# Performance work log

Measured on AMD Instinct MI355X. Metric: run time of the kernel, lower is better.

## Reference

```python
import jax, jax.numpy as jnp
import numpy as np

B, N, C = 16, 577, 768
H = 12
HD = C // H            # 64 head dim
F = HD // 2            # 32 rotary frequency pairs
END = 24               # sqrt(N - 1): patch grid side
SCALE = HD ** -0.5


def setup_inputs() -> dict:
    key = jax.random.key(0)
    k0, k1, k2, k3 = jax.random.split(key, 4)
    x = jax.random.normal(k0, (B, N, C), jnp.float32)
    qkv_w = jax.random.normal(k1, (3 * C, C), jnp.float32) * 0.02
    proj_w = jax.random.normal(k2, (C, C), jnp.float32) * 0.02
    proj_b = jnp.zeros((C,), jnp.float32)
    # learnable mixed 2D RoPE frequencies, [2, H*F] as in init_2d_freqs().view(2,-1)
    freqs = jax.random.normal(k3, (2, H * F), jnp.float32) * 0.5
    return {"x": x, "qkv_w": qkv_w, "proj_w": proj_w, "proj_b": proj_b, "freqs": freqs}


def _rope_angles(freqs):
    # compute_mixed_cis: per-head angle = t_x*fx + t_y*fy over the 24x24 grid
    t = jnp.arange(END * END, dtype=jnp.float32)
    t_x = t % END
    t_y = jnp.floor(t / END)
    ang = t_x[:, None] * freqs[0][None, :] + t_y[:, None] * freqs[1][None, :]  # [Np, H*F]
    return ang.reshape(END * END, H, F).transpose(1, 0, 2)  # [H, Np, F]


def _apply_rope(q, cos, sin):
    # q: [B,H,Np,HD] viewed as complex pairs [B,H,Np,F,2]; rotate by e^{i*ang}
    qp = q.reshape(*q.shape[:-1], F, 2)
    re, im = qp[..., 0], qp[..., 1]
    out = jnp.stack([re * cos - im * sin, re * sin + im * cos], axis=-1)
    return out.reshape(q.shape)


def reference(x, qkv_w, proj_w, proj_b, freqs):
    qkv = (x @ qkv_w.T).reshape(B, N, 3, H, HD).transpose(2, 0, 3, 1, 4)
    q, k, v = qkv[0], qkv[1], qkv[2]              # each [B,H,N,HD]
    ang = _rope_angles(freqs)                      # [H, Np, F]
    cos = jnp.cos(ang)[None]                       # [1,H,Np,F]
    sin = jnp.sin(ang)[None]
    # CLS token (index 0) bypasses RoPE
    q = jnp.concatenate([q[:, :, :1], _apply_rope(q[:, :, 1:], cos, sin)], axis=2)
    k = jnp.concatenate([k[:, :, :1], _apply_rope(k[:, :, 1:], cos, sin)], axis=2)
    attn = jax.nn.softmax((q * SCALE) @ jnp.swapaxes(k, -2, -1), axis=-1)  # [B,H,N,N]
    out = (attn @ v).transpose(0, 2, 1, 3).reshape(B, N, C)
    return out @ proj_w.T + proj_b
```

## Files before the change

### kernel.cpp

```cpp
#include <hip/hip_runtime.h>


typedef __bf16 bf16;
typedef __bf16 bf16x4 __attribute__((ext_vector_type(4)));
typedef __bf16 bf16x8 __attribute__((ext_vector_type(8)));
typedef float f32x4 __attribute__((ext_vector_type(4)));

namespace {
constexpr int kC = 768;
constexpr int kNtok = 577;
constexpr int kM = 16 * kNtok;
constexpr int kMpadQ = 9408;
constexpr int kMpadP = 9344;
constexpr int kTok = 640;
constexpr int kBH = 192;
}

typedef __attribute__((address_space(3))) unsigned int as3_u32;
typedef __attribute__((address_space(1))) unsigned int as1_u32;
__device__ __forceinline__ void gl16(const bf16* g, bf16* l) {
  __builtin_amdgcn_global_load_lds((const as1_u32*)g, (as3_u32*)l, 16, 0, 0);
}

__device__ __forceinline__ int swz_lid(int hid, int nwg) {
  int q = nwg >> 3, r = nwg & 7;
  int x = hid & 7, y = hid >> 3;
  int base = (x < r) ? x * (q + 1) : r * (q + 1) + (x - r) * q;
  return base + y;
}

__global__ __launch_bounds__(256) void prep_kernel(
    const float* __restrict__ x, const float* __restrict__ qkv_w,
    const float* __restrict__ proj_w, const float* __restrict__ freqs,
    bf16* __restrict__ xb, bf16* __restrict__ wqb, bf16* __restrict__ pwb,
    float* __restrict__ cosT, float* __restrict__ sinT) {
  const int bidx = (int)blockIdx.x;
  const int tid = (int)threadIdx.x;
  if (bidx < 3528) {
    int idx = bidx * 256 + tid;
    int m = idx / 96, c8 = (idx % 96) * 8;
    bf16x8 o;
    if (m < kM) {
      const float* p = x + (size_t)m * kC + c8;
#pragma unroll
      for (int j = 0; j < 8; ++j) o[j] = (bf16)p[j];
    } else {
#pragma unroll
      for (int j = 0; j < 8; ++j) o[j] = (bf16)0.0f;
    }
    *(bf16x8*)(xb + (size_t)m * kC + c8) = o;
  } else if (bidx < 3528 + 864) {
    int off = ((bidx - 3528) * 256 + tid) * 8;
    bf16x8 o;
#pragma unroll
    for (int j = 0; j < 8; ++j) o[j] = (bf16)qkv_w[off + j];
    *(bf16x8*)(wqb + off) = o;
  } else if (bidx < 3528 + 864 + 288) {
    int off = ((bidx - 3528 - 864) * 256 + tid) * 8;
    bf16x8 o;
#pragma unroll
    for (int j = 0; j < 8; ++j) o[j] = (bf16)proj_w[off + j];
    *(bf16x8*)(pwb + off) = o;
  } else {
    int idx = (bidx - 3528 - 864 - 288) * 256 + tid;
    int f = idx & 31;
    int t = (idx >> 5) % 576;
    int h = idx / (576 * 32);
    float ang = (float)(t % 24) * freqs[h * 32 + f] + (float)(t / 24) * freqs[384 + h * 32 + f];
    float s, c;
    sincosf(ang, &s, &c);
    cosT[idx] = c;
    sinT[idx] = s;
  }
}

__global__ __launch_bounds__(512, 4) void qkv_gemm_kernel(
    const bf16* __restrict__ xb, const bf16* __restrict__ wb,
    const float* __restrict__ cosT, const float* __restrict__ sinT,
    bf16* __restrict__ qh, bf16* __restrict__ kbq, bf16* __restrict__ vtb) {
  __shared__ __align__(16) char smem[81920];
  bf16* AsB = (bf16*)smem;
  bf16* BsB = (bf16*)(smem + 49152);
  const int tid = (int)threadIdx.x;
  const int l = tid & 63, w = tid >> 6;
  const int lr = l & 15, lg = l >> 4;
  const int wr = (w & 3) * 48, wc = (w >> 2) * 64;

  const int lid = swz_lid((int)blockIdx.x, 49 * 18);
  const int n0 = (lid % 18) * 128, m0 = (lid / 18) * 192;

  const int srow = w * 8 + (l >> 3);
  const int gch = (l & 7) ^ ((l >> 3) & 7);
  const bf16* aG = xb + (size_t)(m0 + srow) * kC + gch * 8;
  const bf16* bG = wb + (size_t)(n0 + srow) * kC + gch * 8;

  f32x4 acc[3][4];
  const f32x4 z = {0.f, 0.f, 0.f, 0.f};
#pragma unroll
  for (int mi = 0; mi < 3; ++mi)
#pragma unroll
    for (int ni = 0; ni < 4; ++ni) acc[mi][ni] = z;

  auto STAGE = [&](int buf, int k0) {
#pragma unroll
    for (int i = 0; i < 3; ++i)
      gl16(aG + (size_t)i * 64 * kC + k0, &AsB[buf * 12288 + (i * 64 + w * 8) * 64]);
#pragma unroll
    for (int j = 0; j < 2; ++j)
      gl16(bG + (size_t)j * 64 * kC + k0, &BsB[buf * 8192 + (j * 64 + w * 8) * 64]);
  };
  auto COMPUTE = [&](int buf) {
    __builtin_amdgcn_s_setprio(1);
#pragma unroll
    for (int kc = 0; kc < 2; ++kc) {
      bf16x8 af[3], bfr[4];
#pragma unroll
      for (int ni = 0; ni < 4; ++ni) {
        int row = wc + ni * 16 + lr;
        bfr[ni] = *(const bf16x8*)&BsB[buf * 8192 + row * 64 + (((kc * 4 + lg) ^ (lr & 7)) << 3)];
      }
#pragma unroll
      for (int mi = 0; mi < 3; ++mi) {
        int row = wr + mi * 16 + lr;
        af[mi] = *(const bf16x8*)&AsB[buf * 12288 + row * 64 + (((kc * 4 + lg) ^ (lr & 7)) << 3)];
      }
#pragma unroll
      for (int mi = 0; mi < 3; ++mi)
#pragma unroll
        for (int ni = 0; ni < 4; ++ni)
          acc[mi][ni] = __builtin_amdgcn_mfma_f32_16x16x32_bf16(af[mi], bfr[ni], acc[mi][ni], 0, 0, 0);
    }
    __builtin_amdgcn_s_setprio(0);
  };

  STAGE(0, 0);
#pragma unroll 1
  for (int t = 0; t < 11; ++t) {
    const int buf = t & 1;
    STAGE(buf ^ 1, (t + 1) * 64);
    asm volatile("s_waitcnt vmcnt(5)" ::: "memory");
    __builtin_amdgcn_sched_barrier(0);
    __builtin_amdgcn_s_barrier();
    COMPUTE(buf);
    __builtin_amdgcn_s_barrier();
    __builtin_amdgcn_sched_barrier(0);
  }
  asm volatile("s_waitcnt vmcnt(0)" ::: "memory");
  __builtin_amdgcn_sched_barrier(0);
  __builtin_amdgcn_s_barrier();
  COMPUTE(1);

  __syncthreads();
  const int which = n0 / kC;
  const int h = ((n0 + wc) % kC) >> 6;

  if (which == 2) {
    bf16* tq = (bf16*)smem + w * 5120;
    const int tokrow = lr;
    const int dl = lg;
#pragma unroll
    for (int mi = 0; mi < 3; ++mi) {
#pragma unroll
      for (int ni = 0; ni < 4; ++ni)
#pragma unroll
        for (int r = 0; r < 4; ++r)
          tq[(lg * 4 + r) * 65 + ni * 16 + lr] = (bf16)acc[mi][ni][r];
      __builtin_amdgcn_sched_barrier(0);
      const int m = m0 + wr + mi * 16 + tokrow;
      if (m < kM) {
        const int b = m / kNtok;
        const int tok = m - b * kNtok;
        bf16* vdst = vtb + ((size_t)(b * 12 + h) * 64 + dl) * kTok + tok;
#pragma unroll
        for (int it = 0; it < 16; ++it)
          vdst[(size_t)(it * 4) * kTok] = tq[tokrow * 65 + it * 4 + dl];
      }
      __builtin_amdgcn_sched_barrier(0);
    }
  } else {
    float* tp = (float*)smem + w * 2560;
    bf16* dst = (which == 0) ? qh : kbq;
    const float sc = (which == 0) ? 0.125f : 1.0f;
    const int c4 = lr * 4;
#pragma unroll
    for (int mi = 0; mi < 3; ++mi) {
#pragma unroll
      for (int ni = 0; ni < 4; ++ni)
#pragma unroll
        for (int r = 0; r < 4; ++r)
          tp[(lg * 4 + r) * 64 + ni * 16 + lr] = acc[mi][ni][r];
      __builtin_amdgcn_sched_barrier(0);
#pragma unroll
      for (int i = 0; i < 4; ++i) {
        const int row = i * 4 + lg;
        const int m = m0 + wr + mi * 16 + row;
        if (m >= kM) continue;
        float4 v4 = *(const float4*)&tp[row * 64 + c4];
        const int b = m / kNtok;
        const int tok = m - b * kNtok;
        float e0 = v4.x, o0 = v4.y, e1 = v4.z, o1 = v4.w;
        if (tok > 0) {
          const int tb = (h * 576 + tok - 1) * 32 + (c4 >> 1);
          float2 cc = *(const float2*)&cosT[tb];
          float2 ss = *(const float2*)&sinT[tb];
          float r0 = e0 * cc.x - o0 * ss.x, i0 = e0 * ss.x + o0 * cc.x;
          float r1 = e1 * cc.y - o1 * ss.y, i1 = e1 * ss.y + o1 * cc.y;
          e0 = r0; o0 = i0; e1 = r1; o1 = i1;
        }
        bf16x4 ov;
        ov[0] = (bf16)(e0 * sc); ov[1] = (bf16)(o0 * sc);
        ov[2] = (bf16)(e1 * sc); ov[3] = (bf16)(o1 * sc);
        *(bf16x4*)(dst + (((size_t)(b * 12 + h)) * kTok + tok) * 64 + c4) = ov;
      }
      __builtin_amdgcn_sched_barrier(0);
    }
  }
}

__global__ __launch_bounds__(512, 8) void attn_kernel(
    const bf16* __restrict__ qh, const bf16* __restrict__ kbq, const bf16* __restrict__ vtb,
    bf16* __restrict__ aoh) {
  __shared__ __align__(16) bf16 Ks[2][64 * 64];
  __shared__ __align__(16) bf16 Vs[2][64 * 64];
  __shared__ __align__(16) bf16 Ps[8][16 * 64];
  const int tid = (int)threadIdx.x;
  const int l = tid & 63, w = tid >> 6;
  const int lr = l & 15, lg = l >> 4;

  const int lid = swz_lid((int)blockIdx.x, 5 * kBH);
  const int bh = lid / 5, qt = lid - bh * 5;
  const int q0 = qt * 128;

  const int srow = w * 8 + (l >> 3);
  const int gch = (l & 7) ^ ((l >> 3) & 7);
  const bf16* kG = kbq + ((size_t)bh * kTok + srow) * 64 + gch * 8;
  const bf16* vG = vtb + ((size_t)bh * 64 + srow) * kTok + gch * 8;

  auto STAGE = [&](int buf, int j0) {
    gl16(kG + (size_t)j0 * 64, &Ks[buf][(w * 8) * 64]);
    gl16(vG + j0, &Vs[buf][(w * 8) * 64]);
  };

  bf16x8 qf[2];
  {
    const bf16* qp = qh + ((size_t)bh * kTok + (q0 + w * 16 + lr)) * 64 + lg * 8;
    qf[0] = *(const bf16x8*)qp;
    qf[1] = *(const bf16x8*)(qp + 32);
  }
  bf16x8 ones;
#pragma unroll
  for (int j = 0; j < 8; ++j) ones[j] = (bf16)1.0f;

  const f32x4 z = {0.f, 0.f, 0.f, 0.f};
  f32x4 o[4];
#pragma unroll
  for (int nf = 0; nf < 4; ++nf) o[nf] = z;
  f32x4 den = z;

  STAGE(0, 0);
#pragma unroll 1
  for (int jt = 0; jt < 9; ++jt) {
    const int cur = jt & 1;
    __syncthreads();
    if (jt < 8) STAGE(cur ^ 1, (jt + 1) * 64);

    f32x4 s[4];
#pragma unroll
    for (int ni = 0; ni < 4; ++ni) s[ni] = z;
    __builtin_amdgcn_s_setprio(1);
#pragma unroll
    for (int kc = 0; kc < 2; ++kc) {
#pragma unroll
      for (int ni = 0; ni < 4; ++ni) {
        int row = ni * 16 + lr;
        bf16x8 kf = *(const bf16x8*)&Ks[cur][row * 64 + (((kc * 4 + lg) ^ (row & 7)) << 3)];
        s[ni] = __builtin_amdgcn_mfma_f32_16x16x32_bf16(qf[kc], kf, s[ni], 0, 0, 0);
      }
    }
    __builtin_amdgcn_s_setprio(0);

#pragma unroll
    for (int ni = 0; ni < 4; ++ni)
#pragma unroll
      for (int r = 0; r < 4; ++r) {
        float p = __expf(s[ni][r]);
        int prow = lg * 4 + r;
        int pcol = ni * 16 + lr;
        Ps[w][prow * 64 + ((((pcol >> 3) ^ (prow & 7)) & 7) << 3) + (pcol & 7)] = (bf16)p;
      }

    __builtin_amdgcn_s_setprio(1);
#pragma unroll
    for (int kc = 0; kc < 2; ++kc) {
      bf16x8 pf = *(const bf16x8*)&Ps[w][lr * 64 + (((kc * 4 + lg) ^ (lr & 7)) << 3)];
      den = __builtin_amdgcn_mfma_f32_16x16x32_bf16(pf, ones, den, 0, 0, 0);
#pragma unroll
      for (int nf = 0; nf < 4; ++nf) {
        int row = nf * 16 + lr;
        bf16x8 vf = *(const bf16x8*)&Vs[cur][row * 64 + (((kc * 4 + lg) ^ (row & 7)) << 3)];
        o[nf] = __builtin_amdgcn_mfma_f32_16x16x32_bf16(pf, vf, o[nf], 0, 0, 0);
      }
    }
    __builtin_amdgcn_s_setprio(0);
  }

  {
    const bf16* k576 = kbq + ((size_t)bh * kTok + 576) * 64;
    bf16x8 ka = *(const bf16x8*)(k576 + lg * 8);
    bf16x8 kb2 = *(const bf16x8*)(k576 + 32 + lg * 8);
    float part = 0.f;
#pragma unroll
    for (int j = 0; j < 8; ++j)
      part += (float)qf[0][j] * (float)ka[j] + (float)qf[1][j] * (float)kb2[j];
    part += __shfl_xor(part, 16);
    part += __shfl_xor(part, 32);
    float v576[4];
#pragma unroll
    for (int nf = 0; nf < 4; ++nf)
      v576[nf] = (float)vtb[((size_t)bh * 64 + nf * 16 + lr) * kTok + 576];
#pragma unroll
    for (int r = 0; r < 4; ++r) {
      float p = __expf(__shfl(part, lg * 4 + r));
      den[r] += p;
#pragma unroll
      for (int nf = 0; nf < 4; ++nf) o[nf][r] += p * v576[nf];
    }
  }

  const int b = bh / 12, h = bh % 12;
#pragma unroll
  for (int r = 0; r < 4; ++r) {
    const int tok = q0 + w * 16 + lg * 4 + r;
    if (tok > 576) continue;
    const float inv = 1.0f / den[r];
    const size_t rowb = ((size_t)(b * kNtok + tok)) * kC + h * 64;
#pragma unroll
    for (int nf = 0; nf < 4; ++nf)
      aoh[rowb + nf * 16 + lr] = (bf16)(o[nf][r] * inv);
  }
}

__global__ __launch_bounds__(512, 4) void proj_gemm_kernel(
    const bf16* __restrict__ ah, const bf16* __restrict__ bw,
    const float* __restrict__ bias, float* __restrict__ out) {
  __shared__ __align__(16) char smem[65536];
  bf16* AsB = (bf16*)smem;
  bf16* BsB = (bf16*)(smem + 32768);
  const int tid = (int)threadIdx.x;
  const int l = tid & 63, w = tid >> 6;
  const int lr = l & 15, lg = l >> 4;
  const int wr = (w & 3) * 32, wc = (w >> 2) * 64;

  const int lid = swz_lid((int)blockIdx.x, 6 * 73);
  const int n0 = (lid % 6) * 128, m0 = (lid / 6) * 128;

  const int srow = w * 16 + (l >> 3);
  const int gch = (l & 7) ^ ((l >> 3) & 7);
  const bf16* aG = ah + (size_t)(m0 + srow) * kC + gch * 8;
  const bf16* bG = bw + (size_t)(n0 + srow) * kC + gch * 8;

  f32x4 acc[2][4];
  const f32x4 z = {0.f, 0.f, 0.f, 0.f};
#pragma unroll
  for (int mi = 0; mi < 2; ++mi)
#pragma unroll
    for (int ni = 0; ni < 4; ++ni) acc[mi][ni] = z;

  auto STAGE = [&](int buf, int k0) {
#pragma unroll
    for (int i = 0; i < 2; ++i) {
      gl16(aG + (size_t)i * 8 * kC + k0, &AsB[buf * 8192 + (w * 16 + i * 8) * 64]);
      gl16(bG + (size_t)i * 8 * kC + k0, &BsB[buf * 8192 + (w * 16 + i * 8) * 64]);
    }
  };
  auto COMPUTE = [&](int buf) {
    __builtin_amdgcn_s_setprio(1);
#pragma unroll
    for (int kc = 0; kc < 2; ++kc) {
      bf16x8 af[2], bfr[4];
#pragma unroll
      for (int ni = 0; ni < 4; ++ni) {
        int row = wc + ni * 16 + lr;
        bfr[ni] = *(const bf16x8*)&BsB[buf * 8192 + row * 64 + (((kc * 4 + lg) ^ (lr & 7)) << 3)];
      }
#pragma unroll
      for (int mi = 0; mi < 2; ++mi) {
        int row = wr + mi * 16 + lr;
        af[mi] = *(const bf16x8*)&AsB[buf * 8192 + row * 64 + (((kc * 4 + lg) ^ (lr & 7)) << 3)];
      }
#pragma unroll
      for (int mi = 0; mi < 2; ++mi)
#pragma unroll
        for (int ni = 0; ni < 4; ++ni)
          acc[mi][ni] = __builtin_amdgcn_mfma_f32_16x16x32_bf16(af[mi], bfr[ni], acc[mi][ni], 0, 0, 0);
    }
    __builtin_amdgcn_s_setprio(0);
  };

  STAGE(0, 0);
#pragma unroll 1
  for (int t = 0; t < 11; ++t) {
    const int buf = t & 1;
    STAGE(buf ^ 1, (t + 1) * 64);
    asm volatile("s_waitcnt vmcnt(4)" ::: "memory");
    __builtin_amdgcn_sched_barrier(0);
    __builtin_amdgcn_s_barrier();
    COMPUTE(buf);
    __builtin_amdgcn_s_barrier();
    __builtin_amdgcn_sched_barrier(0);
  }
  asm volatile("s_waitcnt vmcnt(0)" ::: "memory");
  __builtin_amdgcn_sched_barrier(0);
  __builtin_amdgcn_s_barrier();
  COMPUTE(1);

  __syncthreads();
  float* tp = (float*)smem + w * 2048;
#pragma unroll
  for (int mi = 0; mi < 2; ++mi)
#pragma unroll
    for (int ni = 0; ni < 4; ++ni)
#pragma unroll
      for (int r = 0; r < 4; ++r)
        tp[(mi * 16 + lg * 4 + r) * 64 + ni * 16 + lr] = acc[mi][ni][r];

  const int c4 = lr * 4;
  const int ncol = n0 + wc + c4;
  float4 bv = *(const float4*)&bias[ncol];
#pragma unroll
  for (int i = 0; i < 8; ++i) {
    const int row = i * 4 + lg;
    const int m = m0 + wr + row;
    if (m >= kM) continue;
    float4 v4 = *(const float4*)&tp[row * 64 + c4];
    v4.x += bv.x; v4.y += bv.y; v4.z += bv.z; v4.w += bv.w;
    *(float4*)(out + (size_t)m * kC + ncol) = v4;
  }
}

extern "C" void kernel_launch(void* const* d_in, const int* in_sizes, int n_in,
                              void* d_out, int out_size, void* d_ws, size_t ws_size,
                              hipStream_t stream) {
  const float* x = (const float*)d_in[0];
  const float* qkv_w = (const float*)d_in[1];
  const float* proj_w = (const float*)d_in[2];
  const float* proj_b = (const float*)d_in[3];
  const float* freqs = (const float*)d_in[4];
  float* out = (float*)d_out;

  char* p = (char*)d_ws;
  auto take = [&](size_t bytes) { char* r = p; p += (bytes + 255) & ~(size_t)255; return r; };
  float* cosT = (float*)take(221184 * 4);
  float* sinT = (float*)take(221184 * 4);
  bf16* xb   = (bf16*)take((size_t)kMpadQ * kC * 2);
  bf16* wqb  = (bf16*)take((size_t)2304 * kC * 2);
  bf16* pwb  = (bf16*)take((size_t)kC * kC * 2);
  bf16* qh   = (bf16*)take((size_t)kBH * kTok * 64 * 2);
  bf16* kbq  = (bf16*)take((size_t)kBH * kTok * 64 * 2);
  bf16* vtb  = (bf16*)take((size_t)kBH * 64 * kTok * 2);
  bf16* aoh  = (bf16*)take((size_t)kMpadP * kC * 2);

  prep_kernel<<<3528 + 864 + 288 + 864, 256, 0, stream>>>(
      x, qkv_w, proj_w, freqs, xb, wqb, pwb, cosT, sinT);
  qkv_gemm_kernel<<<dim3(49 * 18), 512, 0, stream>>>(xb, wqb, cosT, sinT, qh, kbq, vtb);
  attn_kernel<<<dim3(5 * kBH), 512, 0, stream>>>(qh, kbq, vtb, aoh);
  proj_gemm_kernel<<<dim3(6 * 73), 512, 0, stream>>>(aoh, pwb, proj_b, out);
}
```

Baseline: 110.4 us.

## Pass softmax probabilities between MFMAs via lane shuffles instead of LDS

The S tile is now computed transposed (K as the A operand), and the exponentiated probabilities are packed to bf16 pairs and redistributed across lanes with xor-16 and xor-32 shuffles. This builds the A-operand fragments for the PV MFMA directly in registers. The per-wave Ps LDS buffer, its scattered stores and its reloads are removed, and launch bounds drop from 8 to 4 blocks per CU. The shuffles add cross-lane traffic and register pressure, and the relaxed occupancy hint may change register allocation and occupancy.

```diff
diff --git a/kernel.cpp b/kernel.cpp
--- a/kernel.cpp
+++ b/kernel.cpp
@@ -2,9 +2,11 @@
 
 
 typedef __bf16 bf16;
+typedef __bf16 bf16x2 __attribute__((ext_vector_type(2)));
 typedef __bf16 bf16x4 __attribute__((ext_vector_type(4)));
 typedef __bf16 bf16x8 __attribute__((ext_vector_type(8)));
 typedef float f32x4 __attribute__((ext_vector_type(4)));
+typedef unsigned int u32x4 __attribute__((ext_vector_type(4)));
 
 namespace {
 constexpr int kC = 768;
@@ -217,12 +219,11 @@
   }
 }
 
-__global__ __launch_bounds__(512, 8) void attn_kernel(
+__global__ __launch_bounds__(512, 4) void attn_kernel(
     const bf16* __restrict__ qh, const bf16* __restrict__ kbq, const bf16* __restrict__ vtb,
     bf16* __restrict__ aoh) {
   __shared__ __align__(16) bf16 Ks[2][64 * 64];
   __shared__ __align__(16) bf16 Vs[2][64 * 64];
-  __shared__ __align__(16) bf16 Ps[8][16 * 64];
   const int tid = (int)threadIdx.x;
   const int l = tid & 63, w = tid >> 6;
   const int lr = l & 15, lg = l >> 4;
@@ -256,6 +257,8 @@
 #pragma unroll
   for (int nf = 0; nf < 4; ++nf) o[nf] = z;
   f32x4 den = z;
+  const bool odd = (lg & 1) != 0;
+  const bool hi2 = (lg >> 1) != 0;
 
   STAGE(0, 0);
 #pragma unroll 1
@@ -274,31 +277,53 @@
       for (int ni = 0; ni < 4; ++ni) {
         int row = ni * 16 + lr;
         bf16x8 kf = *(const bf16x8*)&Ks[cur][row * 64 + (((kc * 4 + lg) ^ (row & 7)) << 3)];
-        s[ni] = __builtin_amdgcn_mfma_f32_16x16x32_bf16(qf[kc], kf, s[ni], 0, 0, 0);
+        s[ni] = __builtin_amdgcn_mfma_f32_16x16x32_bf16(kf, qf[kc], s[ni], 0, 0, 0);
       }
     }
     __builtin_amdgcn_s_setprio(0);
 
-#pragma unroll
-    for (int ni = 0; ni < 4; ++ni)
-#pragma unroll
-      for (int r = 0; r < 4; ++r) {
-        float p = __expf(s[ni][r]);
-        int prow = lg * 4 + r;
-        int pcol = ni * 16 + lr;
-        Ps[w][prow * 64 + ((((pcol >> 3) ^ (prow & 7)) & 7) << 3) + (pcol & 7)] = (bf16)p;
-      }
+    unsigned int Aw[4], Bw[4], Xw[4], Yw[4];
+#pragma unroll
+    for (int n = 0; n < 4; ++n) {
+      bf16x2 pa, pb;
+      pa[0] = (bf16)__expf(s[n][0]); pa[1] = (bf16)__expf(s[n][1]);
+      pb[0] = (bf16)__expf(s[n][2]); pb[1] = (bf16)__expf(s[n][3]);
+      Aw[n] = __builtin_bit_cast(unsigned int, pa);
+      Bw[n] = __builtin_bit_cast(unsigned int, pb);
+      Xw[n] = __shfl_xor(Aw[n], 16);
+      Yw[n] = __shfl_xor(Bw[n], 16);
+    }
+    unsigned int pw[4][4];
+#pragma unroll
+    for (int n = 0; n < 4; ++n) {
+      pw[n][0] = odd ? Xw[n] : Aw[n];
+      pw[n][1] = odd ? Yw[n] : Bw[n];
+      pw[n][2] = odd ? Aw[n] : Xw[n];
+      pw[n][3] = odd ? Bw[n] : Yw[n];
+    }
+    bf16x8 pf2[2];
+#pragma unroll
+    for (int kc = 0; kc < 2; ++kc) {
+      u32x4 wv;
+#pragma unroll
+      for (int i = 0; i < 4; ++i) {
+        unsigned int send = hi2 ? pw[2 * kc][i] : pw[2 * kc + 1][i];
+        unsigned int recv = __shfl_xor(send, 32);
+        unsigned int own = hi2 ? pw[2 * kc + 1][i] : pw[2 * kc][i];
+        wv[i] = (hi2 != odd) ? recv : own;
+      }
+      pf2[kc] = __builtin_bit_cast(bf16x8, wv);
+    }
 
     __builtin_amdgcn_s_setprio(1);
 #pragma unroll
     for (int kc = 0; kc < 2; ++kc) {
-      bf16x8 pf = *(const bf16x8*)&Ps[w][lr * 64 + (((kc * 4 + lg) ^ (lr & 7)) << 3)];
-      den = __builtin_amdgcn_mfma_f32_16x16x32_bf16(pf, ones, den, 0, 0, 0);
+      den = __builtin_amdgcn_mfma_f32_16x16x32_bf16(pf2[kc], ones, den, 0, 0, 0);
 #pragma unroll
       for (int nf = 0; nf < 4; ++nf) {
         int row = nf * 16 + lr;
         bf16x8 vf = *(const bf16x8*)&Vs[cur][row * 64 + (((kc * 4 + lg) ^ (row & 7)) << 3)];
-        o[nf] = __builtin_amdgcn_mfma_f32_16x16x32_bf16(pf, vf, o[nf], 0, 0, 0);
+        o[nf] = __builtin_amdgcn_mfma_f32_16x16x32_bf16(pf2[kc], vf, o[nf], 0, 0, 0);
       }
     }
     __builtin_amdgcn_s_setprio(0);
```

Result: no change. 111.7 us (+1.2%).
